# Kernel tuning notes

Hardware: AMD Instinct MI355X
Metric: run time of the kernel (lower is better)

Reference implementation:

```python
import jax, jax.numpy as jnp
import numpy as np

DIM = 1024
H = 16
HD = DIM // H  # 64
EPS = 1e-6
B, N = 1, 2048


def setup_inputs() -> dict:
    key = jax.random.key(0)
    k1, k2, k3 = jax.random.split(key, 3)
    x = jax.random.normal(k1, (B, N, DIM), dtype=jnp.float32)
    qkv_w = jax.random.normal(k2, (3 * DIM, DIM), dtype=jnp.float32) * 0.02
    proj_w = jax.random.normal(k3, (DIM, DIM), dtype=jnp.float32) * 0.02
    alpha_log = jnp.zeros((H,), dtype=jnp.float32)  # torch init: zeros
    beta_log = jnp.zeros((H,), dtype=jnp.float32)
    return {"x": x, "qkv_w": qkv_w, "proj_w": proj_w,
            "alpha_log": alpha_log, "beta_log": beta_log}


def reference(x, qkv_w, proj_w, alpha_log, beta_log):
    b, n, c = x.shape
    # fused qkv projection (nn.Linear: y = x @ W.T), split into per-head q,k,v
    qkv = (x @ qkv_w.T).reshape(b, n, 3, H, HD).transpose(2, 0, 3, 1, 4)
    q, k, v = qkv[0], qkv[1], qkv[2]  # each [b,h,n,d]
    # positive ReLU feature map
    phi_q = jax.nn.relu(q) + EPS
    phi_k = jax.nn.relu(k) + EPS
    # causal prefix-sum of outer products phi_k v^T -> running state S_n
    kv = jnp.einsum('bhnd,bhne->bhnde', phi_k, v)   # [b,h,n,d,d]
    S = jnp.cumsum(kv, axis=2)                       # prefix sums over n
    out = jnp.einsum('bhnd,bhnde->bhne', phi_q, S)   # [b,h,n,d]
    # SteLLA normalization: per-head alpha'*beta'*sqrt(d) * prefix length
    alpha_p = jax.nn.softplus(alpha_log) + 1e-6
    beta_p = jax.nn.softplus(beta_log) + 1e-6
    scale = (alpha_p * beta_p * jnp.sqrt(jnp.float32(HD))).reshape(1, H, 1, 1)
    pos = jnp.arange(1, n + 1, dtype=x.dtype).reshape(1, 1, n, 1)
    denom = jnp.maximum(scale * pos, EPS)
    out = out / denom
    out = out.transpose(0, 2, 1, 3).reshape(b, n, c)
    return out @ proj_w.T  # output projection (dropout=0 -> identity)
```

## Files before the change

kernel.cpp:

```cpp
#include <hip/hip_runtime.h>
#include <math.h>

#define DIM 1024
#define NH 16
#define HD 64
#define SEQ 2048
#define CHUNK 128
#define NCHUNK (SEQ / CHUNK)
#define QKV_COLS (3 * DIM)

typedef __attribute__((ext_vector_type(8))) short bf16x8;
typedef __attribute__((ext_vector_type(4))) float f32x4;

__device__ __forceinline__ unsigned short f2bf(float f) {
  unsigned int u = __float_as_uint(f);
  u += 0x7FFF + ((u >> 16) & 1);
  return (unsigned short)(u >> 16);
}
__device__ __forceinline__ float bf2f(unsigned short s) {
  return __uint_as_float(((unsigned int)s) << 16);
}
__device__ __forceinline__ int swzb(int byte, int row) {
  return byte ^ ((row & 7) << 4);
}

__global__ __launch_bounds__(256) void convert_all(const float* __restrict__ x,
                                                   const float* __restrict__ qw,
                                                   const float* __restrict__ pw,
                                                   unsigned short* __restrict__ xb,
                                                   unsigned short* __restrict__ qwb,
                                                   unsigned short* __restrict__ pwb) {
  const int b = blockIdx.x;
  const float* in; unsigned short* out; int i;
  if (b < 2048)      { in = x;  out = xb;  i = b * 256 + threadIdx.x; }
  else if (b < 5120) { in = qw; out = qwb; i = (b - 2048) * 256 + threadIdx.x; }
  else               { in = pw; out = pwb; i = (b - 5120) * 256 + threadIdx.x; }
  float4 v = reinterpret_cast<const float4*>(in)[i];
  ushort4 o;
  o.x = f2bf(v.x); o.y = f2bf(v.y); o.z = f2bf(v.z); o.w = f2bf(v.w);
  reinterpret_cast<ushort4*>(out)[i] = o;
}

template <int BM, int BN, int NBUF, bool PHI, typename OutT>
__global__ __launch_bounds__(256) void gemmN_bt(const unsigned short* __restrict__ A,
                                                const unsigned short* __restrict__ W,
                                                OutT* __restrict__ C,
                                                int M, int Nn, int K) {
  constexpr int BK = 32;
  constexpr int MFR = BM / 32;
  constexpr int NFR = BN / 32;
  constexpr int ACH = BM / 64;
  constexpr int BCH = BN / 64;
  constexpr int L = ACH + BCH;
  static_assert(L == 3, "vmcnt ladder assumes L==3");
  __shared__ unsigned short As[NBUF][BM * BK];
  __shared__ unsigned short Bs[NBUF][BN * BK];
  const int tid  = threadIdx.x;
  const int lane = tid & 63;
  const int wv   = tid >> 6;
  const int row0 = blockIdx.y * BM;
  const int col0 = blockIdx.x * BN;
  const int ln15 = lane & 15;
  const int lhi  = lane >> 4;
  const int wr = (wv >> 1) * (BM / 2);
  const int wc = (wv & 1) * (BN / 2);

  f32x4 acc[MFR][NFR] = {};

  auto stage = [&](int buf, int t) {
    const int k0 = t * BK;
#pragma unroll
    for (int tt = 0; tt < ACH; ++tt) {
      const int chunk = wv * ACH + tt;
      const int lid = chunk * 64 + lane;
      const int r  = lid >> 2;
      const int ke = (lid & 3) << 3;
      __builtin_amdgcn_global_load_lds(
          (const __attribute__((address_space(1))) void*)&A[(size_t)(row0 + r) * K + k0 + ke],
          (__attribute__((address_space(3))) void*)&As[buf][chunk * 512], 16, 0, 0);
    }
#pragma unroll
    for (int tt = 0; tt < BCH; ++tt) {
      const int chunk = wv * BCH + tt;
      const int lid = chunk * 64 + lane;
      const int r  = lid >> 2;
      const int ke = (lid & 3) << 3;
      __builtin_amdgcn_global_load_lds(
          (const __attribute__((address_space(1))) void*)&W[(size_t)(col0 + r) * K + k0 + ke],
          (__attribute__((address_space(3))) void*)&Bs[buf][chunk * 512], 16, 0, 0);
    }
  };

  const int nt = K / BK;
#pragma unroll
  for (int i = 0; i < NBUF - 1; ++i) stage(i, i);
  for (int t = 0; t < nt; ++t) {
    const int k = (nt - 1 - t) < (NBUF - 2) ? (nt - 1 - t) : (NBUF - 2);
    switch (k) {
      case 4:  asm volatile("s_waitcnt vmcnt(12)" ::: "memory"); break;
      case 3:  asm volatile("s_waitcnt vmcnt(9)"  ::: "memory"); break;
      case 2:  asm volatile("s_waitcnt vmcnt(6)"  ::: "memory"); break;
      case 1:  asm volatile("s_waitcnt vmcnt(3)"  ::: "memory"); break;
      default: asm volatile("s_waitcnt vmcnt(0)"  ::: "memory"); break;
    }
    __builtin_amdgcn_s_barrier();
    if (t + NBUF - 1 < nt) stage((t + NBUF - 1) % NBUF, t + NBUF - 1);
    const int cur = t % NBUF;
    bf16x8 a[MFR], b[NFR];
#pragma unroll
    for (int m = 0; m < MFR; ++m)
      a[m] = *reinterpret_cast<const bf16x8*>(&As[cur][(wr + m * 16 + ln15) * BK + lhi * 8]);
#pragma unroll
    for (int n = 0; n < NFR; ++n)
      b[n] = *reinterpret_cast<const bf16x8*>(&Bs[cur][(wc + n * 16 + ln15) * BK + lhi * 8]);
#pragma unroll
    for (int m = 0; m < MFR; ++m)
#pragma unroll
      for (int n = 0; n < NFR; ++n)
        acc[m][n] = __builtin_amdgcn_mfma_f32_16x16x32_bf16(a[m], b[n], acc[m][n], 0, 0, 0);
  }

  const int crow = lhi * 4;
  const int ccol = ln15;
#pragma unroll
  for (int m = 0; m < MFR; ++m)
#pragma unroll
    for (int n = 0; n < NFR; ++n)
#pragma unroll
      for (int r = 0; r < 4; ++r) {
        const int gc = col0 + wc + n * 16 + ccol;
        float v = acc[m][n][r];
        if constexpr (PHI) {
          if (gc < 2 * DIM) v = fmaxf(v, 0.f) + 1e-6f;
        }
        const size_t idx = (size_t)(row0 + wr + m * 16 + crow + r) * Nn + gc;
        if constexpr (sizeof(OutT) == 2) C[idx] = (OutT)f2bf(v);
        else                             C[idx] = v;
      }
}

__global__ __launch_bounds__(256) void ckv_mfma_kernel(const unsigned short* __restrict__ qkv,
                                                       float* __restrict__ ckv) {
  const int h = blockIdx.x / NCHUNK;
  const int c = blockIdx.x % NCHUNK;
  const int tid  = threadIdx.x;
  const int lane = tid & 63;
  const int w    = tid >> 6;
  const int ln15 = lane & 15;
  const int lhi  = lane >> 4;

  __shared__ unsigned short kst[HD * CHUNK];
  __shared__ unsigned short vt[HD * CHUNK];

  for (int i = tid; i < CHUNK * HD / 4; i += 256) {
    const int r = i >> 4;
    const int d4 = (i & 15) << 2;
    const size_t base = (size_t)(c * CHUNK + r) * QKV_COLS + h * HD + d4;
    ushort4 k4 = *reinterpret_cast<const ushort4*>(&qkv[base + DIM]);
    ushort4 v4 = *reinterpret_cast<const ushort4*>(&qkv[base + 2 * DIM]);
#pragma unroll
    for (int j = 0; j < 4; ++j) {
      const int d = d4 + j;
      *reinterpret_cast<unsigned short*>((char*)kst + swzb(d * 256 + r * 2, d)) = (&k4.x)[j];
      *reinterpret_cast<unsigned short*>((char*)vt + swzb(d * 256 + r * 2, d)) = (&v4.x)[j];
    }
  }
  __syncthreads();

  f32x4 acc[4] = {};
#pragma unroll
  for (int ks = 0; ks < 4; ++ks) {
    const int dr = w * 16 + ln15;
    bf16x8 a = *reinterpret_cast<const bf16x8*>((char*)kst + swzb(dr * 256 + (ks * 32 + lhi * 8) * 2, dr));
#pragma unroll
    for (int et = 0; et < 4; ++et) {
      const int er = et * 16 + ln15;
      bf16x8 b = *reinterpret_cast<const bf16x8*>((char*)vt + swzb(er * 256 + (ks * 32 + lhi * 8) * 2, er));
      acc[et] = __builtin_amdgcn_mfma_f32_16x16x32_bf16(a, b, acc[et], 0, 0, 0);
    }
  }
  const size_t base = (size_t)(h * NCHUNK + c) * (HD * HD);
#pragma unroll
  for (int et = 0; et < 4; ++et)
#pragma unroll
    for (int r = 0; r < 4; ++r)
      ckv[base + (size_t)(w * 16 + lhi * 4 + r) * HD + et * 16 + ln15] = acc[et][r];
}

__global__ __launch_bounds__(256) void attn_mfma_kernel(const unsigned short* __restrict__ qkv,
                                                        const float* __restrict__ ckv,
                                                        const float* __restrict__ alpha_log,
                                                        const float* __restrict__ beta_log,
                                                        unsigned short* __restrict__ attn_out) {
  const int h = blockIdx.x / NCHUNK;
  const int c = blockIdx.x % NCHUNK;
  const int tid  = threadIdx.x;
  const int lane = tid & 63;
  const int w    = tid >> 6;
  const int ln15 = lane & 15;
  const int lhi  = lane >> 4;

  __shared__ unsigned short ks[CHUNK * HD];
  __shared__ unsigned short vst[HD * 256];
  __shared__ unsigned short ps[CHUNK * CHUNK];

  float sp[16];
#pragma unroll
  for (int p = 0; p < 16; ++p) sp[p] = 0.f;
  {
    const float* cb = ckv + (size_t)h * NCHUNK * (HD * HD) + tid * 16;
    for (int cc = 0; cc < c; ++cc) {
      const float4* p4 = reinterpret_cast<const float4*>(cb + (size_t)cc * (HD * HD));
#pragma unroll
      for (int q = 0; q < 4; ++q) {
        float4 t = p4[q];
        sp[q * 4 + 0] += t.x; sp[q * 4 + 1] += t.y;
        sp[q * 4 + 2] += t.z; sp[q * 4 + 3] += t.w;
      }
    }
  }
  {
    const int d = tid >> 2;
#pragma unroll
    for (int j = 0; j < 16; ++j) {
      const int e = (tid & 3) * 16 + j;
      const float sv = sp[j];
      const unsigned short hi = f2bf(sv);
      const unsigned short lo = f2bf(sv - bf2f(hi));
      *reinterpret_cast<unsigned short*>((char*)vst + swzb(e * 512 + d * 2, e)) = hi;
      *reinterpret_cast<unsigned short*>((char*)vst + swzb(e * 512 + (64 + d) * 2, e)) = lo;
    }
  }

  for (int i = tid; i < CHUNK * HD / 4; i += 256) {
    const int r = i >> 4;
    const int d4 = (i & 15) << 2;
    const size_t base = (size_t)(c * CHUNK + r) * QKV_COLS + h * HD + d4;
    ushort4 k4 = *reinterpret_cast<const ushort4*>(&qkv[base + DIM]);
    ushort4 v4 = *reinterpret_cast<const ushort4*>(&qkv[base + 2 * DIM]);
    *reinterpret_cast<ushort4*>((char*)ks + swzb(r * 128 + d4 * 2, r)) = k4;
#pragma unroll
    for (int j = 0; j < 4; ++j) {
      const int e = d4 + j;
      *reinterpret_cast<unsigned short*>((char*)vst + swzb(e * 512 + (128 + r) * 2, e)) = (&v4.x)[j];
    }
  }
  bf16x8 qf[2][2];
#pragma unroll
  for (int m = 0; m < 2; ++m)
#pragma unroll
    for (int kk = 0; kk < 2; ++kk) {
      const size_t gq = (size_t)(c * CHUNK + w * 32 + m * 16 + ln15) * QKV_COLS
                        + h * HD + kk * 32 + lhi * 8;
      qf[m][kk] = *reinterpret_cast<const bf16x8*>(&qkv[gq]);
    }
  __syncthreads();

  f32x4 accs[2][8] = {};
#pragma unroll
  for (int j = 0; j < 8; ++j) {
    const int col = j * 16 + ln15;
    bf16x8 b0 = *reinterpret_cast<const bf16x8*>((char*)ks + swzb(col * 128 + lhi * 16, col));
    bf16x8 b1 = *reinterpret_cast<const bf16x8*>((char*)ks + swzb(col * 128 + 64 + lhi * 16, col));
#pragma unroll
    for (int m = 0; m < 2; ++m) {
      accs[m][j] = __builtin_amdgcn_mfma_f32_16x16x32_bf16(qf[m][0], b0, accs[m][j], 0, 0, 0);
      accs[m][j] = __builtin_amdgcn_mfma_f32_16x16x32_bf16(qf[m][1], b1, accs[m][j], 0, 0, 0);
    }
  }
#pragma unroll
  for (int m = 0; m < 2; ++m)
#pragma unroll
    for (int j = 0; j < 8; ++j)
#pragma unroll
      for (int r = 0; r < 4; ++r) {
        const int qrow = w * 32 + m * 16 + lhi * 4 + r;
        const int kcol = j * 16 + ln15;
        const float val = (qrow >= kcol) ? accs[m][j][r] : 0.f;
        *reinterpret_cast<unsigned short*>((char*)ps + swzb(qrow * 256 + kcol * 2, qrow)) = f2bf(val);
      }
  __syncthreads();

  f32x4 acco[2][4] = {};
#pragma unroll
  for (int kk = 0; kk < 8; ++kk) {
    bf16x8 a[2];
    if (kk < 4) {
#pragma unroll
      for (int m = 0; m < 2; ++m) a[m] = qf[m][kk & 1];
    } else {
#pragma unroll
      for (int m = 0; m < 2; ++m) {
        const int row = w * 32 + m * 16 + ln15;
        a[m] = *reinterpret_cast<const bf16x8*>((char*)ps + swzb(row * 256 + (kk - 4) * 64 + lhi * 16, row));
      }
    }
#pragma unroll
    for (int ct = 0; ct < 4; ++ct) {
      const int e = ct * 16 + ln15;
      bf16x8 b = *reinterpret_cast<const bf16x8*>((char*)vst + swzb(e * 512 + kk * 64 + lhi * 16, e));
#pragma unroll
      for (int m = 0; m < 2; ++m)
        acco[m][ct] = __builtin_amdgcn_mfma_f32_16x16x32_bf16(a[m], b, acco[m][ct], 0, 0, 0);
    }
  }

  const float ap = log1pf(expf(alpha_log[h])) + 1e-6f;
  const float bp = log1pf(expf(beta_log[h])) + 1e-6f;
  const float scale = ap * bp * 8.0f;
#pragma unroll
  for (int m = 0; m < 2; ++m)
#pragma unroll
    for (int ct = 0; ct < 4; ++ct)
#pragma unroll
      for (int r = 0; r < 4; ++r) {
        const int n = c * CHUNK + w * 32 + m * 16 + lhi * 4 + r;
        const float inv = 1.0f / fmaxf(scale * (float)(n + 1), 1e-6f);
        attn_out[(size_t)n * DIM + h * HD + ct * 16 + ln15] = f2bf(acco[m][ct][r] * inv);
      }
}

extern "C" void kernel_launch(void* const* d_in, const int* in_sizes, int n_in,
                              void* d_out, int out_size, void* d_ws, size_t ws_size,
                              hipStream_t stream) {
  const float* x        = (const float*)d_in[0];
  const float* qkv_w    = (const float*)d_in[1];
  const float* proj_w   = (const float*)d_in[2];
  const float* alpha_lg = (const float*)d_in[3];
  const float* beta_lg  = (const float*)d_in[4];
  float* out = (float*)d_out;

  char* ws = (char*)d_ws;
  size_t off = 0;
  unsigned short* qkvb = (unsigned short*)(ws + off); off += (size_t)SEQ * QKV_COLS * 2;
  float*          ckv  = (float*)         (ws + off); off += (size_t)NH * NCHUNK * HD * HD * 4;
  unsigned short* attn = (unsigned short*)(ws + off); off += (size_t)SEQ * DIM * 2;
  unsigned short* xb   = (unsigned short*)(ws + off); off += (size_t)SEQ * DIM * 2;
  unsigned short* qwb  = (unsigned short*)(ws + off); off += (size_t)QKV_COLS * DIM * 2;
  unsigned short* pwb  = (unsigned short*)(ws + off); off += (size_t)DIM * DIM * 2;

  convert_all<<<6144, 256, 0, stream>>>(x, qkv_w, proj_w, xb, qwb, pwb);
  gemmN_bt<64, 128, 4, true, unsigned short><<<dim3(QKV_COLS / 128, SEQ / 64), 256, 0, stream>>>(
      xb, qwb, qkvb, SEQ, QKV_COLS, DIM);
  ckv_mfma_kernel<<<NH * NCHUNK, 256, 0, stream>>>(qkvb, ckv);
  attn_mfma_kernel<<<NH * NCHUNK, 256, 0, stream>>>(qkvb, ckv, alpha_lg, beta_lg, attn);
  gemmN_bt<128, 64, 6, false, float><<<dim3(DIM / 64, SEQ / 128), 256, 0, stream>>>(
      attn, pwb, out, SEQ, DIM, DIM);
}
```

Measured before the change: 76.09 us.

## Fuse chunk-state and attention kernels using inter-block flag synchronization

Merges the per-chunk KV state kernel and the attention kernel into one launch. Each block computes its own chunk's K^T V, publishes it to global memory with a release flag, then waits on the flags of earlier chunks of the same head before summing their states. K/V are loaded once into shared memory and reused by both phases, with the transposed K staged in the P buffer. This removes one kernel launch and one reload of K/V, but adds a memset launch and relies on all earlier-chunk blocks being resident or already scheduled to avoid spin-wait stalls.

```diff
diff --git a/kernel.cpp b/kernel.cpp
--- a/kernel.cpp
+++ b/kernel.cpp
@@ -139,8 +139,12 @@
       }
 }
 
-__global__ __launch_bounds__(256) void ckv_mfma_kernel(const unsigned short* __restrict__ qkv,
-                                                       float* __restrict__ ckv) {
+__global__ __launch_bounds__(256) void attn_fused_kernel(const unsigned short* __restrict__ qkv,
+                                                         float* __restrict__ ckv,
+                                                         unsigned int* __restrict__ flags,
+                                                         const float* __restrict__ alpha_log,
+                                                         const float* __restrict__ beta_log,
+                                                         unsigned short* __restrict__ attn_out) {
   const int h = blockIdx.x / NCHUNK;
   const int c = blockIdx.x % NCHUNK;
   const int tid  = threadIdx.x;
@@ -149,8 +153,10 @@
   const int ln15 = lane & 15;
   const int lhi  = lane >> 4;
 
-  __shared__ unsigned short kst[HD * CHUNK];
-  __shared__ unsigned short vt[HD * CHUNK];
+  __shared__ unsigned short ks[CHUNK * HD];
+  __shared__ unsigned short vst[HD * 256];
+  __shared__ unsigned short ps[CHUNK * CHUNK];
+  unsigned short* kst = ps;
 
   for (int i = tid; i < CHUNK * HD / 4; i += 256) {
     const int r = i >> 4;
@@ -158,56 +164,60 @@
     const size_t base = (size_t)(c * CHUNK + r) * QKV_COLS + h * HD + d4;
     ushort4 k4 = *reinterpret_cast<const ushort4*>(&qkv[base + DIM]);
     ushort4 v4 = *reinterpret_cast<const ushort4*>(&qkv[base + 2 * DIM]);
+    *reinterpret_cast<ushort4*>((char*)ks + swzb(r * 128 + d4 * 2, r)) = k4;
 #pragma unroll
     for (int j = 0; j < 4; ++j) {
       const int d = d4 + j;
       *reinterpret_cast<unsigned short*>((char*)kst + swzb(d * 256 + r * 2, d)) = (&k4.x)[j];
-      *reinterpret_cast<unsigned short*>((char*)vt + swzb(d * 256 + r * 2, d)) = (&v4.x)[j];
-    }
-  }
-  __syncthreads();
-
-  f32x4 acc[4] = {};
-#pragma unroll
-  for (int ks = 0; ks < 4; ++ks) {
+      *reinterpret_cast<unsigned short*>((char*)vst + swzb(d * 512 + (128 + r) * 2, d)) = (&v4.x)[j];
+    }
+  }
+  bf16x8 qf[2][2];
+#pragma unroll
+  for (int m = 0; m < 2; ++m)
+#pragma unroll
+    for (int kk = 0; kk < 2; ++kk) {
+      const size_t gq = (size_t)(c * CHUNK + w * 32 + m * 16 + ln15) * QKV_COLS
+                        + h * HD + kk * 32 + lhi * 8;
+      qf[m][kk] = *reinterpret_cast<const bf16x8*>(&qkv[gq]);
+    }
+  __syncthreads();
+
+  {
+    f32x4 cacc[4] = {};
     const int dr = w * 16 + ln15;
-    bf16x8 a = *reinterpret_cast<const bf16x8*>((char*)kst + swzb(dr * 256 + (ks * 32 + lhi * 8) * 2, dr));
-#pragma unroll
-    for (int et = 0; et < 4; ++et) {
-      const int er = et * 16 + ln15;
-      bf16x8 b = *reinterpret_cast<const bf16x8*>((char*)vt + swzb(er * 256 + (ks * 32 + lhi * 8) * 2, er));
-      acc[et] = __builtin_amdgcn_mfma_f32_16x16x32_bf16(a, b, acc[et], 0, 0, 0);
-    }
-  }
-  const size_t base = (size_t)(h * NCHUNK + c) * (HD * HD);
-#pragma unroll
-  for (int et = 0; et < 4; ++et)
-#pragma unroll
-    for (int r = 0; r < 4; ++r)
-      ckv[base + (size_t)(w * 16 + lhi * 4 + r) * HD + et * 16 + ln15] = acc[et][r];
-}
-
-__global__ __launch_bounds__(256) void attn_mfma_kernel(const unsigned short* __restrict__ qkv,
-                                                        const float* __restrict__ ckv,
-                                                        const float* __restrict__ alpha_log,
-                                                        const float* __restrict__ beta_log,
-                                                        unsigned short* __restrict__ attn_out) {
-  const int h = blockIdx.x / NCHUNK;
-  const int c = blockIdx.x % NCHUNK;
-  const int tid  = threadIdx.x;
-  const int lane = tid & 63;
-  const int w    = tid >> 6;
-  const int ln15 = lane & 15;
-  const int lhi  = lane >> 4;
-
-  __shared__ unsigned short ks[CHUNK * HD];
-  __shared__ unsigned short vst[HD * 256];
-  __shared__ unsigned short ps[CHUNK * CHUNK];
-
-  float sp[16];
-#pragma unroll
-  for (int p = 0; p < 16; ++p) sp[p] = 0.f;
+#pragma unroll
+    for (int ksl = 0; ksl < 4; ++ksl) {
+      bf16x8 a = *reinterpret_cast<const bf16x8*>((char*)kst + swzb(dr * 256 + (ksl * 32 + lhi * 8) * 2, dr));
+#pragma unroll
+      for (int et = 0; et < 4; ++et) {
+        const int er = et * 16 + ln15;
+        bf16x8 b = *reinterpret_cast<const bf16x8*>((char*)vst + swzb(er * 512 + (128 + ksl * 32 + lhi * 8) * 2, er));
+        cacc[et] = __builtin_amdgcn_mfma_f32_16x16x32_bf16(a, b, cacc[et], 0, 0, 0);
+      }
+    }
+    const size_t base = (size_t)(h * NCHUNK + c) * (HD * HD);
+#pragma unroll
+    for (int et = 0; et < 4; ++et)
+#pragma unroll
+      for (int r = 0; r < 4; ++r)
+        ckv[base + (size_t)(w * 16 + lhi * 4 + r) * HD + et * 16 + ln15] = cacc[et][r];
+  }
+  __threadfence();
+  __syncthreads();
+  if (tid == 0)
+    __hip_atomic_store(&flags[h * NCHUNK + c], 1u, __ATOMIC_RELEASE, __HIP_MEMORY_SCOPE_AGENT);
+
+  if (tid < c) {
+    while (__hip_atomic_load(&flags[h * NCHUNK + tid], __ATOMIC_ACQUIRE, __HIP_MEMORY_SCOPE_AGENT) == 0u)
+      __builtin_amdgcn_s_sleep(1);
+    __threadfence();
+  }
+  __syncthreads();
   {
+    float sp[16];
+#pragma unroll
+    for (int p = 0; p < 16; ++p) sp[p] = 0.f;
     const float* cb = ckv + (size_t)h * NCHUNK * (HD * HD) + tid * 16;
     for (int cc = 0; cc < c; ++cc) {
       const float4* p4 = reinterpret_cast<const float4*>(cb + (size_t)cc * (HD * HD));
@@ -218,8 +228,6 @@
         sp[q * 4 + 2] += t.z; sp[q * 4 + 3] += t.w;
       }
     }
-  }
-  {
     const int d = tid >> 2;
 #pragma unroll
     for (int j = 0; j < 16; ++j) {
@@ -231,29 +239,6 @@
       *reinterpret_cast<unsigned short*>((char*)vst + swzb(e * 512 + (64 + d) * 2, e)) = lo;
     }
   }
-
-  for (int i = tid; i < CHUNK * HD / 4; i += 256) {
-    const int r = i >> 4;
-    const int d4 = (i & 15) << 2;
-    const size_t base = (size_t)(c * CHUNK + r) * QKV_COLS + h * HD + d4;
-    ushort4 k4 = *reinterpret_cast<const ushort4*>(&qkv[base + DIM]);
-    ushort4 v4 = *reinterpret_cast<const ushort4*>(&qkv[base + 2 * DIM]);
-    *reinterpret_cast<ushort4*>((char*)ks + swzb(r * 128 + d4 * 2, r)) = k4;
-#pragma unroll
-    for (int j = 0; j < 4; ++j) {
-      const int e = d4 + j;
-      *reinterpret_cast<unsigned short*>((char*)vst + swzb(e * 512 + (128 + r) * 2, e)) = (&v4.x)[j];
-    }
-  }
-  bf16x8 qf[2][2];
-#pragma unroll
-  for (int m = 0; m < 2; ++m)
-#pragma unroll
-    for (int kk = 0; kk < 2; ++kk) {
-      const size_t gq = (size_t)(c * CHUNK + w * 32 + m * 16 + ln15) * QKV_COLS
-                        + h * HD + kk * 32 + lhi * 8;
-      qf[m][kk] = *reinterpret_cast<const bf16x8*>(&qkv[gq]);
-    }
   __syncthreads();
 
   f32x4 accs[2][8] = {};
@@ -338,12 +323,13 @@
   unsigned short* xb   = (unsigned short*)(ws + off); off += (size_t)SEQ * DIM * 2;
   unsigned short* qwb  = (unsigned short*)(ws + off); off += (size_t)QKV_COLS * DIM * 2;
   unsigned short* pwb  = (unsigned short*)(ws + off); off += (size_t)DIM * DIM * 2;
+  unsigned int*   flags = (unsigned int*) (ws + off); off += (size_t)NH * NCHUNK * 4;
 
   convert_all<<<6144, 256, 0, stream>>>(x, qkv_w, proj_w, xb, qwb, pwb);
   gemmN_bt<64, 128, 4, true, unsigned short><<<dim3(QKV_COLS / 128, SEQ / 64), 256, 0, stream>>>(
       xb, qwb, qkvb, SEQ, QKV_COLS, DIM);
-  ckv_mfma_kernel<<<NH * NCHUNK, 256, 0, stream>>>(qkvb, ckv);
-  attn_mfma_kernel<<<NH * NCHUNK, 256, 0, stream>>>(qkvb, ckv, alpha_lg, beta_lg, attn);
+  hipMemsetAsync(flags, 0, NH * NCHUNK * sizeof(unsigned int), stream);
+  attn_fused_kernel<<<NH * NCHUNK, 256, 0, stream>>>(qkvb, ckv, flags, alpha_lg, beta_lg, attn);
   gemmN_bt<128, 64, 6, false, float><<<dim3(DIM / 64, SEQ / 128), 256, 0, stream>>>(
       attn, pwb, out, SEQ, DIM, DIM);
 }
```

After: 109.7 us. 44.2% more time.
